# Kernel optimization log

Hardware: AMD Instinct MI355X
Metric: run time of the kernel (lower is better)

## Reference

```python
import jax, jax.numpy as jnp
import numpy as np

HEADS = 24
HEAD_DIM = 128
DIM = HEADS * HEAD_DIM  # 3072
EPS = 1e-6


def setup_inputs() -> dict:
    key = jax.random.key(0)
    ks = jax.random.split(key, 10)
    B, S_IMG, S_TXT = 1, 2048, 256
    hidden_states = jax.random.normal(ks[0], (B, S_IMG, DIM), jnp.float32)
    encoder_hidden_states = jax.random.normal(ks[1], (B, S_TXT, DIM), jnp.float32)
    # RoPE tables for image tokens, interleaved pair layout [S_IMG, HEAD_DIM]
    inv = 1.0 / (10000.0 ** (np.arange(0, HEAD_DIM, 2, dtype=np.float32) / HEAD_DIM))
    ang = np.arange(S_IMG, dtype=np.float32)[:, None] * inv[None, :]  # [S, Dh/2]
    ang = np.repeat(ang, 2, axis=-1)  # [S, Dh], pairs (2i, 2i+1) share angle
    rope_cos = jnp.asarray(np.cos(ang), jnp.float32)
    rope_sin = jnp.asarray(np.sin(ang), jnp.float32)
    s = 0.02
    wq = jax.random.normal(ks[2], (DIM, DIM), jnp.float32) * s
    wk = jax.random.normal(ks[3], (DIM, DIM), jnp.float32) * s
    wv = jax.random.normal(ks[4], (DIM, DIM), jnp.float32) * s
    wo = jax.random.normal(ks[5], (DIM, DIM), jnp.float32) * s
    bq = jax.random.normal(ks[6], (DIM,), jnp.float32) * s
    bk = jax.random.normal(ks[7], (DIM,), jnp.float32) * s
    bv = jax.random.normal(ks[8], (DIM,), jnp.float32) * s
    bo = jax.random.normal(ks[9], (DIM,), jnp.float32) * s
    norm_q_w = jnp.ones((HEAD_DIM,), jnp.float32)
    norm_k_w = jnp.ones((HEAD_DIM,), jnp.float32)
    return dict(hidden_states=hidden_states, encoder_hidden_states=encoder_hidden_states,
                rope_cos=rope_cos, rope_sin=rope_sin,
                wq=wq, bq=bq, wk=wk, bk=bk, wv=wv, bv=bv,
                norm_q_w=norm_q_w, norm_k_w=norm_k_w, wo=wo, bo=bo)


def _rmsnorm(x, w):
    var = jnp.mean(jnp.square(x), axis=-1, keepdims=True)
    return x * jax.lax.rsqrt(var + EPS) * w


def _rope(x, cos, sin):
    # x [B,H,S,Dh]; diffusers apply_rotary_emb with use_real_unbind_dim=-1:
    # pairs are interleaved (x[2i], x[2i+1]) -> rotated = stack(-imag, real)
    xr = x[..., 0::2]
    xi = x[..., 1::2]
    x_rot = jnp.stack([-xi, xr], axis=-1).reshape(x.shape)
    return x * cos + x_rot * sin


def reference(hidden_states, encoder_hidden_states, rope_cos, rope_sin,
              wq, bq, wk, bk, wv, bv, norm_q_w, norm_k_w, wo, bo):
    B, s_img, D = hidden_states.shape
    s_txt = encoder_hidden_states.shape[1]
    S = s_img + s_txt
    x = jnp.concatenate([hidden_states, encoder_hidden_states], axis=1)  # [B,S,D]

    def proj(w, b):
        return (x @ w + b).reshape(B, S, HEADS, HEAD_DIM).transpose(0, 2, 1, 3)  # [B,H,S,Dh]

    q = _rmsnorm(proj(wq, bq), norm_q_w)
    k = _rmsnorm(proj(wk, bk), norm_k_w)
    v = proj(wv, bv)
    # RoPE on image tokens only
    q = jnp.concatenate([_rope(q[:, :, :s_img], rope_cos, rope_sin), q[:, :, s_img:]], axis=2)
    k = jnp.concatenate([_rope(k[:, :, :s_img], rope_cos, rope_sin), k[:, :, s_img:]], axis=2)
    scale = 1.0 / jnp.sqrt(jnp.float32(HEAD_DIM))
    scores = jnp.einsum('bhqd,bhkd->bhqk', q, k) * scale
    attn = jax.nn.softmax(scores, axis=-1)
    out = jnp.einsum('bhqk,bhkd->bhqd', attn, v)
    out = out.transpose(0, 2, 1, 3).reshape(B, S, D)
    img = out[:, :s_img] @ wo + bo  # to_out[0]; to_out[1] is Dropout(p=0) -> identity
    txt = out[:, s_img:]            # to_add_out is None in this branch
    return img, txt
```

## Files before the change

kernel.cpp:

```cpp
#include <hip/hip_runtime.h>
#include <cstdint>

typedef __bf16 bf16_t;
typedef bf16_t bf16x8 __attribute__((ext_vector_type(8)));
typedef bf16_t bf16x4 __attribute__((ext_vector_type(4)));
typedef float  floatx4 __attribute__((ext_vector_type(4)));

#define S_ALL 2304
#define SIMG  2048
#define NH    24
#define HD    128
#define DIM   3072
#define NQKV  9216

#define SHIFT2 17.312340490667562f
#define QSCALE 0.12751744f

typedef __attribute__((address_space(1))) void* gp1_t;
typedef __attribute__((address_space(3))) void* lp3_t;

__device__ __forceinline__ void async16(const void* g, void* l) {
    __builtin_amdgcn_global_load_lds((gp1_t)(g), (lp3_t)(l), 16, 0, 0);
}
__device__ __forceinline__ floatx4 mfma_bf16(bf16x8 a, bf16x8 b, floatx4 c) {
    return __builtin_amdgcn_mfma_f32_16x16x32_bf16(a, b, c, 0, 0, 0);
}

__global__ __launch_bounds__(256) void k_convert_x(const float* __restrict__ hid,
                                                   const float* __restrict__ enc,
                                                   bf16_t* __restrict__ xb) {
    long i = ((long)blockIdx.x * 256 + threadIdx.x) * 4;
    const long HN = (long)SIMG * DIM;
    float4 f = (i < HN) ? *(const float4*)(hid + i) : *(const float4*)(enc + (i - HN));
    bf16x4 o;
    o[0] = (bf16_t)f.x; o[1] = (bf16_t)f.y; o[2] = (bf16_t)f.z; o[3] = (bf16_t)f.w;
    *(bf16x4*)(xb + i) = o;
}

__global__ __launch_bounds__(256) void k_wT4(const float* __restrict__ wq, const float* __restrict__ wk,
                                             const float* __restrict__ wv, const float* __restrict__ wo,
                                             bf16_t* __restrict__ wTq, bf16_t* __restrict__ woT) {
    __shared__ __align__(16) bf16_t T[64][72];
    int z = blockIdx.z;
    const float* W = (z == 0) ? wq : (z == 1) ? wk : (z == 2) ? wv : wo;
    bf16_t* Wt = (z < 3) ? (wTq + (long)z * DIM * DIM) : woT;
    int r0 = blockIdx.x * 64, c0 = blockIdx.y * 64;
    int tid = threadIdx.x;
    int lr = tid >> 2, lc = (tid & 3) * 16;
    const float* src = W + (long)(r0 + lr) * DIM + c0 + lc;
#pragma unroll
    for (int i = 0; i < 16; i += 4) {
        float4 f = *(const float4*)(src + i);
        T[lr][lc + i + 0] = (bf16_t)f.x;
        T[lr][lc + i + 1] = (bf16_t)f.y;
        T[lr][lc + i + 2] = (bf16_t)f.z;
        T[lr][lc + i + 3] = (bf16_t)f.w;
    }
    __syncthreads();
    bf16x8 a, b;
#pragma unroll
    for (int i = 0; i < 8; i++) a[i] = T[lc + i][lr];
#pragma unroll
    for (int i = 0; i < 8; i++) b[i] = T[lc + 8 + i][lr];
    bf16_t* dst = Wt + (long)(c0 + lr) * DIM + r0 + lc;
    *(bf16x8*)dst = a;
    *(bf16x8*)(dst + 8) = b;
}

__global__ __launch_bounds__(256) void k_bias(const float* __restrict__ bq, const float* __restrict__ bk,
                                              const float* __restrict__ bv, float* __restrict__ bcat) {
    int i = blockIdx.x * 256 + threadIdx.x;
    float v = (i < DIM) ? bq[i] : (i < 2 * DIM ? bk[i - DIM] : bv[i - 2 * DIM]);
    bcat[i] = v;
}

__global__ __launch_bounds__(256) void k_gemm_bt(const bf16_t* __restrict__ A,
                                                 const bf16_t* __restrict__ Bt,
                                                 const float* __restrict__ bias,
                                                 bf16_t* __restrict__ Cb, float* __restrict__ Cf,
                                                 int M, int N, int K) {
    __shared__ __align__(16) bf16_t As[128 * 64];
    __shared__ __align__(16) bf16_t Bs[128 * 64];
    int tid = threadIdx.x;
    int wave = tid >> 6, lane = tid & 63;
    int quad = lane >> 4, l16 = lane & 15;
    long m0 = (long)blockIdx.y * 128, n0 = (long)blockIdx.x * 128;
    int wm = (wave >> 1) * 64, wn = (wave & 1) * 64;

    floatx4 zero = {0.f, 0.f, 0.f, 0.f};
    floatx4 acc[4][4];
#pragma unroll
    for (int i = 0; i < 4; i++)
#pragma unroll
        for (int j = 0; j < 4; j++) acc[i][j] = zero;

    int kxor = ((lane & 7) ^ ((lane >> 3) & 7)) * 8;
    const bf16_t* Ag = A + (m0 + wave * 32 + (lane >> 3)) * K + kxor;
    const bf16_t* Bg = Bt + (n0 + wave * 32 + (lane >> 3)) * K + kxor;
    char* AsB = (char*)As + wave * 4096;
    char* BsB = (char*)Bs + wave * 4096;

    for (int k0 = 0; k0 < K; k0 += 64) {
#pragma unroll
        for (int c2 = 0; c2 < 4; ++c2) {
            async16(Ag + (long)c2 * 8 * K + k0, AsB + c2 * 1024);
            async16(Bg + (long)c2 * 8 * K + k0, BsB + c2 * 1024);
        }
        __syncthreads();
#pragma unroll
        for (int ks = 0; ks < 2; ++ks) {
            bf16x8 af[4], bfr[4];
            int ch = 0;
#pragma unroll
            for (int i = 0; i < 4; i++) {
                ch = ((ks * 4 + quad) ^ (l16 & 7)) * 8;
                af[i] = *(const bf16x8*)&As[(wm + i * 16 + l16) * 64 + ch];
            }
#pragma unroll
            for (int i = 0; i < 4; i++)
                bfr[i] = *(const bf16x8*)&Bs[(wn + i * 16 + l16) * 64 + ch];
#pragma unroll
            for (int i = 0; i < 4; i++)
#pragma unroll
                for (int j = 0; j < 4; j++) acc[i][j] = mfma_bf16(af[i], bfr[j], acc[i][j]);
        }
        __syncthreads();
    }

#pragma unroll
    for (int i = 0; i < 4; i++) {
        long rowb = m0 + wm + i * 16 + quad * 4;
#pragma unroll
        for (int j = 0; j < 4; j++) {
            long col = n0 + wn + j * 16 + l16;
            float bv = bias ? bias[col] : 0.0f;
#pragma unroll
            for (int r = 0; r < 4; r++) {
                float v = acc[i][j][r] + bv;
                long idx = (rowb + r) * N + col;
                if (Cb) Cb[idx] = (bf16_t)v;
                else    Cf[idx] = v;
            }
        }
    }
}

__global__ __launch_bounds__(256) void k_qk_epi(const bf16_t* __restrict__ qkvb,
                                                const float* __restrict__ rope_cos,
                                                const float* __restrict__ rope_sin,
                                                const float* __restrict__ nqw,
                                                const float* __restrict__ nkw,
                                                bf16_t* __restrict__ qo, bf16_t* __restrict__ ko) {
    int tid = threadIdx.x, wave = tid >> 6, lane = tid & 63;
    int row_id = blockIdx.x * 4 + wave;
    int t = row_id / (S_ALL * NH);
    int rem = row_id - t * (S_ALL * NH);
    int h = rem / S_ALL;
    int s = rem - h * S_ALL;
    const bf16_t* src = qkvb + (long)s * NQKV + t * DIM + h * HD + lane * 2;
    float x0 = (float)src[0], x1 = (float)src[1];
    float ss = x0 * x0 + x1 * x1;
#pragma unroll
    for (int off = 1; off < 64; off <<= 1) ss += __shfl_xor(ss, off);
    float r = rsqrtf(ss * (1.0f / 128.0f) + 1e-6f);
    const float* w = t ? nkw : nqw;
    x0 *= r * w[lane * 2];
    x1 *= r * w[lane * 2 + 1];
    if (s < SIMG) {
        float c = rope_cos[s * HD + lane * 2];
        float sn = rope_sin[s * HD + lane * 2];
        float y0 = x0 * c - x1 * sn;
        float y1 = x1 * c + x0 * sn;
        x0 = y0; x1 = y1;
    }
    if (t == 0) { x0 *= QSCALE; x1 *= QSCALE; }
    bf16_t* dst = (t ? ko : qo) + (long)h * S_ALL * HD + (long)s * HD + lane * 2;
    dst[0] = (bf16_t)x0;
    dst[1] = (bf16_t)x1;
}

__global__ __launch_bounds__(256) void k_vT(const bf16_t* __restrict__ qkvb, bf16_t* __restrict__ vT) {
    __shared__ __align__(16) bf16_t T[64][72];
    int h = blockIdx.z;
    int s0 = blockIdx.x * 64, d0 = blockIdx.y * 64;
    int tid = threadIdx.x, lr = tid >> 2, lc = (tid & 3) * 16;
    const bf16_t* src = qkvb + (long)(s0 + lr) * NQKV + 2 * DIM + h * HD + d0 + lc;
    bf16x8 a = *(const bf16x8*)src, b = *(const bf16x8*)(src + 8);
#pragma unroll
    for (int i = 0; i < 8; i++) { T[lr][lc + i] = a[i]; T[lr][lc + 8 + i] = b[i]; }
    __syncthreads();
    bf16x8 c, d;
#pragma unroll
    for (int i = 0; i < 8; i++) c[i] = T[lc + i][lr];
#pragma unroll
    for (int i = 0; i < 8; i++) d[i] = T[lc + 8 + i][lr];
    bf16_t* dst = vT + (long)h * HD * S_ALL + (long)(d0 + lr) * S_ALL + s0 + lc;
    *(bf16x8*)dst = c;
    *(bf16x8*)(dst + 8) = d;
}

__global__ __launch_bounds__(256, 2) void k_attn(const bf16_t* __restrict__ q,
                                                 const bf16_t* __restrict__ k,
                                                 const bf16_t* __restrict__ vT,
                                                 bf16_t* __restrict__ ao,
                                                 float* __restrict__ out_txt) {
    __shared__ __align__(16) bf16_t Ks[64 * 128];
    __shared__ __align__(16) bf16_t VTs[128 * 64];
    __shared__ __align__(16) bf16_t Ps[4][2][16 * 64];
    int tid = threadIdx.x, wave = tid >> 6, lane = tid & 63;
    int quad = lane >> 4, l16 = lane & 15;
    int h = blockIdx.y;
    int q0 = blockIdx.x * 128 + wave * 32;
    const long hbase = (long)h * S_ALL * HD;
    const char* kgb = (const char*)(k + hbase);
    const char* vgb = (const char*)(vT + hbase);

    int koffB[4], voffB[4], slotB[4];
#pragma unroll
    for (int c2 = 0; c2 < 4; ++c2) {
        int L = (wave * 4 + c2) * 64 + lane;
        slotB[c2] = L;
        int rk = L >> 4, ck = (L & 15) ^ (rk & 15);
        koffB[c2] = rk * 256 + ck * 16;
        int rv = L >> 3, cv = (L & 7) ^ (rv & 7) ^ (((rv >> 3) & 1) << 2);
        voffB[c2] = rv * (S_ALL * 2) + cv * 16;
    }

    bf16x8 qf[2][4];
#pragma unroll
    for (int st = 0; st < 2; ++st) {
        const bf16_t* qp = q + hbase + (long)(q0 + st * 16 + l16) * HD + quad * 8;
#pragma unroll
        for (int ks = 0; ks < 4; ++ks) qf[st][ks] = *(const bf16x8*)(qp + ks * 32);
    }

    floatx4 zero = {0.f, 0.f, 0.f, 0.f};
    floatx4 o0[8], o1[8];
#pragma unroll
    for (int ni = 0; ni < 8; ++ni) { o0[ni] = zero; o1[ni] = zero; }
    floatx4 lac0 = zero, lac1 = zero;

    for (int kb = 0; kb < S_ALL / 64; ++kb) {
        const char* kg = kgb + (long)kb * 16384;
        const char* vg = vgb + kb * 128;
#pragma unroll
        for (int c2 = 0; c2 < 4; ++c2) {
            async16(kg + koffB[c2], (char*)Ks + slotB[c2] * 16);
            async16(vg + voffB[c2], (char*)VTs + slotB[c2] * 16);
        }
        __syncthreads();

        floatx4 s0[4], s1[4];
#pragma unroll
        for (int ni = 0; ni < 4; ++ni) { s0[ni] = zero; s1[ni] = zero; }
#pragma unroll
        for (int ks = 0; ks < 4; ++ks)
#pragma unroll
            for (int ni = 0; ni < 4; ++ni) {
                int slot = (ni * 16 + l16) * 16 + ((ks * 4 + quad) ^ l16);
                bf16x8 kf = *(const bf16x8*)&Ks[slot * 8];
                s0[ni] = mfma_bf16(qf[0][ks], kf, s0[ni]);
                s1[ni] = mfma_bf16(qf[1][ks], kf, s1[ni]);
            }

#pragma unroll
        for (int st = 0; st < 2; ++st) {
#pragma unroll
            for (int ni = 0; ni < 4; ++ni) {
                floatx4 sv = st ? s1[ni] : s0[ni];
                floatx4 p;
#pragma unroll
                for (int j = 0; j < 4; ++j) p[j] = __builtin_amdgcn_exp2f(sv[j] - SHIFT2);
                if (st) lac1 += p; else lac0 += p;
#pragma unroll
                for (int j = 0; j < 4; ++j) {
                    int r = quad * 4 + j;
                    int chunk = ((ni * 16 + l16) >> 3) ^ ((r >> 1) & 7);
                    Ps[wave][st][r * 64 + chunk * 8 + (l16 & 7)] = (bf16_t)p[j];
                }
            }
        }

        bf16x8 pf[2][2];
#pragma unroll
        for (int st = 0; st < 2; ++st)
#pragma unroll
            for (int k2 = 0; k2 < 2; ++k2) {
                int chunk = (k2 * 4 + quad) ^ ((l16 >> 1) & 7);
                pf[st][k2] = *(const bf16x8*)&Ps[wave][st][l16 * 64 + chunk * 8];
            }

#pragma unroll
        for (int k2 = 0; k2 < 2; ++k2)
#pragma unroll
            for (int ni = 0; ni < 8; ++ni) {
                int r = ni * 16 + l16;
                int c = (k2 * 4 + quad) ^ (l16 & 7) ^ (((l16 >> 3) & 1) << 2);
                bf16x8 vf = *(const bf16x8*)&VTs[r * 64 + c * 8];
                o0[ni] = mfma_bf16(pf[0][k2], vf, o0[ni]);
                o1[ni] = mfma_bf16(pf[1][k2], vf, o1[ni]);
            }
        __syncthreads();
    }

#pragma unroll
    for (int off = 1; off < 16; off <<= 1) {
#pragma unroll
        for (int j = 0; j < 4; ++j) {
            lac0[j] += __shfl_xor(lac0[j], off);
            lac1[j] += __shfl_xor(lac1[j], off);
        }
    }

#pragma unroll
    for (int st = 0; st < 2; ++st) {
#pragma unroll
        for (int j = 0; j < 4; ++j) {
            float rl = 1.0f / (st ? lac1[j] : lac0[j]);
            int s_row = q0 + st * 16 + quad * 4 + j;
#pragma unroll
            for (int ni = 0; ni < 8; ++ni) {
                float v = (st ? o1[ni][j] : o0[ni][j]) * rl;
                int col = h * HD + ni * 16 + l16;
                ao[(long)s_row * DIM + col] = (bf16_t)v;
                if (s_row >= SIMG) out_txt[(long)(s_row - SIMG) * DIM + col] = v;
            }
        }
    }
}

extern "C" void kernel_launch(void* const* d_in, const int* in_sizes, int n_in,
                              void* d_out, int out_size, void* d_ws, size_t ws_size,
                              hipStream_t stream) {
    const float* hid = (const float*)d_in[0];
    const float* enc = (const float*)d_in[1];
    const float* rope_cos = (const float*)d_in[2];
    const float* rope_sin = (const float*)d_in[3];
    const float* wq = (const float*)d_in[4];
    const float* bq = (const float*)d_in[5];
    const float* wk = (const float*)d_in[6];
    const float* bk = (const float*)d_in[7];
    const float* wv = (const float*)d_in[8];
    const float* bv = (const float*)d_in[9];
    const float* nqw = (const float*)d_in[10];
    const float* nkw = (const float*)d_in[11];
    const float* wo = (const float*)d_in[12];
    const float* bo = (const float*)d_in[13];
    float* out = (float*)d_out;

    char* ws = (char*)d_ws;
    bf16_t* xb   = (bf16_t*)(ws);
    bf16_t* wTq  = (bf16_t*)(ws + 14155776L);
    bf16_t* woT  = (bf16_t*)(ws + 70778880L);
    float*  bcat = (float*) (ws + 89653248L);
    bf16_t* qkvb = (bf16_t*)(ws + 89690112L);
    bf16_t* qb   = (bf16_t*)(ws + 132157440L);
    bf16_t* kbuf = (bf16_t*)(ws + 146313216L);
    bf16_t* vT   = (bf16_t*)(ws + 160468992L);
    bf16_t* ao   = (bf16_t*)(ws + 174624768L);

    k_convert_x<<<6912, 256, 0, stream>>>(hid, enc, xb);
    k_wT4<<<dim3(48, 48, 4), 256, 0, stream>>>(wq, wk, wv, wo, wTq, woT);
    k_bias<<<36, 256, 0, stream>>>(bq, bk, bv, bcat);
    k_gemm_bt<<<dim3(72, 18), 256, 0, stream>>>(xb, wTq, bcat, qkvb, (float*)nullptr, S_ALL, NQKV, DIM);
    k_qk_epi<<<27648, 256, 0, stream>>>(qkvb, rope_cos, rope_sin, nqw, nkw, qb, kbuf);
    k_vT<<<dim3(36, 2, 24), 256, 0, stream>>>(qkvb, vT);
    k_attn<<<dim3(18, 24), 256, 0, stream>>>(qb, kbuf, vT, ao, out + (long)SIMG * DIM);
    k_gemm_bt<<<dim3(24, 16), 256, 0, stream>>>(ao, woT, bo, (bf16_t*)nullptr, out, SIMG, DIM, DIM);
}
```

Before: 573.4 us.

## Fuse QKV bias, RMSNorm, RoPE and V transpose into the QKV GEMM epilogue

The QKV projection GEMM now does the per-head bias add, RMSNorm, RoPE, Q scaling and the V transpose in its epilogue. Each 128-column tile maps to exactly one head of Q, K or V, with the row sum of squares reduced across two waves through shared memory. This drops the separate bias, qk-epilogue and V-transpose kernels and the bf16 QKV intermediate round trip through global memory. The cost is a heavier GEMM epilogue with scattered 2-byte stores for Q/K and an extra LDS transpose step for V.

```diff
diff --git a/kernel.cpp b/kernel.cpp
--- a/kernel.cpp
+++ b/kernel.cpp
@@ -67,11 +67,155 @@
     *(bf16x8*)(dst + 8) = b;
 }
 
-__global__ __launch_bounds__(256) void k_bias(const float* __restrict__ bq, const float* __restrict__ bk,
-                                              const float* __restrict__ bv, float* __restrict__ bcat) {
-    int i = blockIdx.x * 256 + threadIdx.x;
-    float v = (i < DIM) ? bq[i] : (i < 2 * DIM ? bk[i - DIM] : bv[i - 2 * DIM]);
-    bcat[i] = v;
+__global__ __launch_bounds__(256) void k_gemm_qkv(const bf16_t* __restrict__ A,
+                                                  const bf16_t* __restrict__ Bt,
+                                                  const float* __restrict__ bq_,
+                                                  const float* __restrict__ bk_,
+                                                  const float* __restrict__ bv_,
+                                                  const float* __restrict__ rope_cos,
+                                                  const float* __restrict__ rope_sin,
+                                                  const float* __restrict__ nqw,
+                                                  const float* __restrict__ nkw,
+                                                  bf16_t* __restrict__ qo,
+                                                  bf16_t* __restrict__ ko,
+                                                  bf16_t* __restrict__ vT) {
+    __shared__ __align__(16) char smem[33 * 1024];
+    bf16_t* As = (bf16_t*)smem;
+    bf16_t* Bs = (bf16_t*)(smem + 16384);
+    float* ssq = (float*)(smem + 32768);
+    int tid = threadIdx.x;
+    int wave = tid >> 6, lane = tid & 63;
+    int quad = lane >> 4, l16 = lane & 15;
+    long m0 = (long)blockIdx.y * 128, n0 = (long)blockIdx.x * 128;
+    int t = blockIdx.x / 24, h = blockIdx.x % 24;
+    int wm = (wave >> 1) * 64, wn = (wave & 1) * 64;
+
+    floatx4 zero = {0.f, 0.f, 0.f, 0.f};
+    floatx4 acc[4][4];
+#pragma unroll
+    for (int i = 0; i < 4; i++)
+#pragma unroll
+        for (int j = 0; j < 4; j++) acc[i][j] = zero;
+
+    int kxor = ((lane & 7) ^ ((lane >> 3) & 7)) * 8;
+    const bf16_t* Ag = A + (m0 + wave * 32 + (lane >> 3)) * DIM + kxor;
+    const bf16_t* Bg = Bt + (n0 + wave * 32 + (lane >> 3)) * DIM + kxor;
+    char* AsB = (char*)As + wave * 4096;
+    char* BsB = (char*)Bs + wave * 4096;
+
+    for (int k0 = 0; k0 < DIM; k0 += 64) {
+#pragma unroll
+        for (int c2 = 0; c2 < 4; ++c2) {
+            async16(Ag + (long)c2 * 8 * DIM + k0, AsB + c2 * 1024);
+            async16(Bg + (long)c2 * 8 * DIM + k0, BsB + c2 * 1024);
+        }
+        __syncthreads();
+#pragma unroll
+        for (int ks = 0; ks < 2; ++ks) {
+            bf16x8 af[4], bfr[4];
+            int ch = ((ks * 4 + quad) ^ (l16 & 7)) * 8;
+#pragma unroll
+            for (int i = 0; i < 4; i++)
+                af[i] = *(const bf16x8*)&As[(wm + i * 16 + l16) * 64 + ch];
+#pragma unroll
+            for (int i = 0; i < 4; i++)
+                bfr[i] = *(const bf16x8*)&Bs[(wn + i * 16 + l16) * 64 + ch];
+#pragma unroll
+            for (int i = 0; i < 4; i++)
+#pragma unroll
+                for (int j = 0; j < 4; j++) acc[i][j] = mfma_bf16(af[i], bfr[j], acc[i][j]);
+        }
+        __syncthreads();
+    }
+
+    int dcol[4];
+#pragma unroll
+    for (int j = 0; j < 4; j++) dcol[j] = wn + j * 16 + l16;
+
+    if (t == 2) {
+        float bias4[4];
+#pragma unroll
+        for (int j = 0; j < 4; j++) bias4[j] = bv_[h * HD + dcol[j]];
+        char* vbuf = smem;
+#pragma unroll
+        for (int i = 0; i < 4; i++)
+#pragma unroll
+            for (int r = 0; r < 4; r++) {
+                int s_l = wm + i * 16 + quad * 4 + r;
+#pragma unroll
+                for (int j = 0; j < 4; j++) {
+                    int d = dcol[j];
+                    int chunk = d * 16 + ((s_l >> 3) ^ (d & 15));
+                    *(bf16_t*)(vbuf + chunk * 16 + (s_l & 7) * 2) = (bf16_t)(acc[i][j][r] + bias4[j]);
+                }
+            }
+        __syncthreads();
+        int d = tid >> 1, sh = tid & 1;
+        bf16_t* dstv = vT + (long)h * HD * S_ALL + (long)d * S_ALL + m0 + sh * 64;
+#pragma unroll
+        for (int k8 = 0; k8 < 8; ++k8) {
+            int s8 = sh * 8 + k8;
+            bf16x8 frag = *(const bf16x8*)(vbuf + (d * 16 + (s8 ^ (d & 15))) * 16);
+            *(bf16x8*)(dstv + k8 * 8) = frag;
+        }
+    } else {
+        const float* bp = t ? bk_ : bq_;
+        const float* nw = t ? nkw : nqw;
+        float bias4[4], wv4[4];
+#pragma unroll
+        for (int j = 0; j < 4; j++) {
+            bias4[j] = bp[h * HD + dcol[j]];
+            wv4[j] = nw[dcol[j]];
+        }
+        int wmh = wm >> 6, wnh = wn >> 6;
+#pragma unroll
+        for (int i = 0; i < 4; i++)
+#pragma unroll
+            for (int r = 0; r < 4; r++) {
+                float s2 = 0.f;
+#pragma unroll
+                for (int j = 0; j < 4; j++) {
+                    float v = acc[i][j][r] + bias4[j];
+                    acc[i][j][r] = v;
+                    s2 += v * v;
+                }
+                s2 += __shfl_xor(s2, 1);
+                s2 += __shfl_xor(s2, 2);
+                s2 += __shfl_xor(s2, 4);
+                s2 += __shfl_xor(s2, 8);
+                if (l16 == 0) ssq[(wmh * 64 + i * 16 + quad * 4 + r) * 2 + wnh] = s2;
+            }
+        __syncthreads();
+        bf16_t* dst = (t ? ko : qo) + (long)h * S_ALL * HD;
+        bool do_rope = (m0 < SIMG);
+#pragma unroll
+        for (int i = 0; i < 4; i++)
+#pragma unroll
+            for (int r = 0; r < 4; r++) {
+                int row = i * 16 + quad * 4 + r;
+                int s_abs = (int)m0 + wm + row;
+                float tot = ssq[(wmh * 64 + row) * 2] + ssq[(wmh * 64 + row) * 2 + 1];
+                float rms = rsqrtf(tot * (1.0f / 128.0f) + 1e-6f);
+                float y[4];
+#pragma unroll
+                for (int j = 0; j < 4; j++) y[j] = acc[i][j][r] * rms * wv4[j];
+                if (do_rope) {
+                    const float* cp = rope_cos + (long)s_abs * HD;
+                    const float* sp = rope_sin + (long)s_abs * HD;
+#pragma unroll
+                    for (int j = 0; j < 4; j++) {
+                        float c = cp[dcol[j]], sn = sp[dcol[j]];
+                        float px = __shfl_xor(y[j], 1);
+                        y[j] = y[j] * c + ((l16 & 1) ? px : -px) * sn;
+                    }
+                }
+#pragma unroll
+                for (int j = 0; j < 4; j++) {
+                    float v = t ? y[j] : y[j] * QSCALE;
+                    dst[(long)s_abs * HD + dcol[j]] = (bf16_t)v;
+                }
+            }
+    }
 }
 
 __global__ __launch_bounds__(256) void k_gemm_bt(const bf16_t* __restrict__ A,
@@ -110,12 +254,10 @@
 #pragma unroll
         for (int ks = 0; ks < 2; ++ks) {
             bf16x8 af[4], bfr[4];
-            int ch = 0;
-#pragma unroll
-            for (int i = 0; i < 4; i++) {
-                ch = ((ks * 4 + quad) ^ (l16 & 7)) * 8;
+            int ch = ((ks * 4 + quad) ^ (l16 & 7)) * 8;
+#pragma unroll
+            for (int i = 0; i < 4; i++)
                 af[i] = *(const bf16x8*)&As[(wm + i * 16 + l16) * 64 + ch];
-            }
 #pragma unroll
             for (int i = 0; i < 4; i++)
                 bfr[i] = *(const bf16x8*)&Bs[(wn + i * 16 + l16) * 64 + ch];
@@ -143,60 +285,6 @@
             }
         }
     }
-}
-
-__global__ __launch_bounds__(256) void k_qk_epi(const bf16_t* __restrict__ qkvb,
-                                                const float* __restrict__ rope_cos,
-                                                const float* __restrict__ rope_sin,
-                                                const float* __restrict__ nqw,
-                                                const float* __restrict__ nkw,
-                                                bf16_t* __restrict__ qo, bf16_t* __restrict__ ko) {
-    int tid = threadIdx.x, wave = tid >> 6, lane = tid & 63;
-    int row_id = blockIdx.x * 4 + wave;
-    int t = row_id / (S_ALL * NH);
-    int rem = row_id - t * (S_ALL * NH);
-    int h = rem / S_ALL;
-    int s = rem - h * S_ALL;
-    const bf16_t* src = qkvb + (long)s * NQKV + t * DIM + h * HD + lane * 2;
-    float x0 = (float)src[0], x1 = (float)src[1];
-    float ss = x0 * x0 + x1 * x1;
-#pragma unroll
-    for (int off = 1; off < 64; off <<= 1) ss += __shfl_xor(ss, off);
-    float r = rsqrtf(ss * (1.0f / 128.0f) + 1e-6f);
-    const float* w = t ? nkw : nqw;
-    x0 *= r * w[lane * 2];
-    x1 *= r * w[lane * 2 + 1];
-    if (s < SIMG) {
-        float c = rope_cos[s * HD + lane * 2];
-        float sn = rope_sin[s * HD + lane * 2];
-        float y0 = x0 * c - x1 * sn;
-        float y1 = x1 * c + x0 * sn;
-        x0 = y0; x1 = y1;
-    }
-    if (t == 0) { x0 *= QSCALE; x1 *= QSCALE; }
-    bf16_t* dst = (t ? ko : qo) + (long)h * S_ALL * HD + (long)s * HD + lane * 2;
-    dst[0] = (bf16_t)x0;
-    dst[1] = (bf16_t)x1;
-}
-
-__global__ __launch_bounds__(256) void k_vT(const bf16_t* __restrict__ qkvb, bf16_t* __restrict__ vT) {
-    __shared__ __align__(16) bf16_t T[64][72];
-    int h = blockIdx.z;
-    int s0 = blockIdx.x * 64, d0 = blockIdx.y * 64;
-    int tid = threadIdx.x, lr = tid >> 2, lc = (tid & 3) * 16;
-    const bf16_t* src = qkvb + (long)(s0 + lr) * NQKV + 2 * DIM + h * HD + d0 + lc;
-    bf16x8 a = *(const bf16x8*)src, b = *(const bf16x8*)(src + 8);
-#pragma unroll
-    for (int i = 0; i < 8; i++) { T[lr][lc + i] = a[i]; T[lr][lc + 8 + i] = b[i]; }
-    __syncthreads();
-    bf16x8 c, d;
-#pragma unroll
-    for (int i = 0; i < 8; i++) c[i] = T[lc + i][lr];
-#pragma unroll
-    for (int i = 0; i < 8; i++) d[i] = T[lc + 8 + i][lr];
-    bf16_t* dst = vT + (long)h * HD * S_ALL + (long)(d0 + lr) * S_ALL + s0 + lc;
-    *(bf16x8*)dst = c;
-    *(bf16x8*)(dst + 8) = d;
 }
 
 __global__ __launch_bounds__(256, 2) void k_attn(const bf16_t* __restrict__ q,
@@ -352,19 +440,15 @@
     bf16_t* xb   = (bf16_t*)(ws);
     bf16_t* wTq  = (bf16_t*)(ws + 14155776L);
     bf16_t* woT  = (bf16_t*)(ws + 70778880L);
-    float*  bcat = (float*) (ws + 89653248L);
-    bf16_t* qkvb = (bf16_t*)(ws + 89690112L);
-    bf16_t* qb   = (bf16_t*)(ws + 132157440L);
-    bf16_t* kbuf = (bf16_t*)(ws + 146313216L);
-    bf16_t* vT   = (bf16_t*)(ws + 160468992L);
-    bf16_t* ao   = (bf16_t*)(ws + 174624768L);
+    bf16_t* qb   = (bf16_t*)(ws + 89653248L);
+    bf16_t* kbuf = (bf16_t*)(ws + 103809024L);
+    bf16_t* vT   = (bf16_t*)(ws + 117964800L);
+    bf16_t* ao   = (bf16_t*)(ws + 132120576L);
 
     k_convert_x<<<6912, 256, 0, stream>>>(hid, enc, xb);
     k_wT4<<<dim3(48, 48, 4), 256, 0, stream>>>(wq, wk, wv, wo, wTq, woT);
-    k_bias<<<36, 256, 0, stream>>>(bq, bk, bv, bcat);
-    k_gemm_bt<<<dim3(72, 18), 256, 0, stream>>>(xb, wTq, bcat, qkvb, (float*)nullptr, S_ALL, NQKV, DIM);
-    k_qk_epi<<<27648, 256, 0, stream>>>(qkvb, rope_cos, rope_sin, nqw, nkw, qb, kbuf);
-    k_vT<<<dim3(36, 2, 24), 256, 0, stream>>>(qkvb, vT);
+    k_gemm_qkv<<<dim3(72, 18), 256, 0, stream>>>(xb, wTq, bq, bk, bv, rope_cos, rope_sin,
+                                                 nqw, nkw, qb, kbuf, vT);
     k_attn<<<dim3(18, 24), 256, 0, stream>>>(qb, kbuf, vT, ao, out + (long)SIMG * DIM);
     k_gemm_bt<<<dim3(24, 16), 256, 0, stream>>>(ao, woT, bo, (bf16_t*)nullptr, out, SIMG, DIM, DIM);
 }
```

Measured after the change: 562.4 us. No clear change (-1.9%).
